# Kernel optimization log

Hardware: AMD Instinct MI355X
Metric: run time of the kernel (lower is better)

The kernel has to match this reference:

```python
import jax, jax.numpy as jnp
import numpy as np
import math

BLK_NUM, BLK_SIZE = 128, 8
DIM, N_HEADS, N_KV_HEADS = 1024, 16, 4
HEAD_DIM = DIM // N_HEADS            # 64
HIDDEN = 64 * ((DIM + 63) // 64)     # 1024 (FeedForward hidden_dim)
BATCH = 4
SEQ = BLK_NUM * BLK_SIZE             # 1024
EPS = 1e-6
ROPE_THETA = 10000.0


def setup_inputs() -> dict:
    key = jax.random.key(0)
    ks = jax.random.split(key, 12)
    std = 1.0 / math.sqrt(DIM)
    f32 = jnp.float32
    inp = {
        "x":   jax.random.normal(ks[0], (BATCH, SEQ, DIM), f32),
        "vec": jax.random.normal(ks[1], (BATCH, BLK_NUM, DIM), f32),
        "wq": jax.random.normal(ks[2], (N_HEADS * HEAD_DIM, DIM), f32) * std,
        "wk": jax.random.normal(ks[3], (N_KV_HEADS * HEAD_DIM, DIM), f32) * std,
        "wv": jax.random.normal(ks[4], (N_KV_HEADS * HEAD_DIM, DIM), f32) * std,
        "wo": jax.random.normal(ks[5], (DIM, N_HEADS * HEAD_DIM), f32) * std,
        "w1": jax.random.normal(ks[6], (HIDDEN, DIM), f32) * std,
        "w2": jax.random.normal(ks[7], (DIM, HIDDEN), f32) * std,
        "w3": jax.random.normal(ks[8], (HIDDEN, DIM), f32) * std,
        "mod_attn_w": jax.random.normal(ks[9], (3 * DIM, DIM), f32) * std,
        "mod_attn_b": jnp.zeros((3 * DIM,), f32),
        "mod_ffn_w":  jax.random.normal(ks[10], (3 * DIM, DIM), f32) * std,
        "mod_ffn_b":  jnp.zeros((3 * DIM,), f32),
        "norm1_w": jnp.ones((DIM,), f32),
        "norm2_w": jnp.ones((DIM,), f32),
    }
    # rotary tables (equivalent to llama-style precompute_freqs_cis, theta=rope_scaling)
    inv_freq = 1.0 / (ROPE_THETA ** (jnp.arange(0, HEAD_DIM, 2, dtype=f32) / HEAD_DIM))
    angles = jnp.outer(jnp.arange(SEQ, dtype=f32), inv_freq)  # (SEQ, HEAD_DIM//2)
    inp["freqs_cos"] = jnp.cos(angles)
    inp["freqs_sin"] = jnp.sin(angles)
    return inp


def _rmsnorm(x, w):
    return x * jax.lax.rsqrt(jnp.mean(x * x, axis=-1, keepdims=True) + EPS) * w


def _rope(x, cos, sin):
    # x: (B, L, H, Dh); pairs are adjacent dims, matching view_as_complex on (..., Dh//2, 2)
    x1, x2 = x[..., 0::2], x[..., 1::2]
    c, s = cos[None, :, None, :], sin[None, :, None, :]
    return jnp.stack([x1 * c - x2 * s, x1 * s + x2 * c], axis=-1).reshape(x.shape)


def _modulate(vec, w, b):
    # adaLN: silu(vec) -> 3*dim, chunked into shift/scale/gate, one vector per block
    out = jax.nn.silu(vec) @ w.T + b
    shift, scale, gate = jnp.split(out, 3, axis=-1)
    rep = lambda t: jnp.repeat(t, BLK_SIZE, axis=1)  # (B, M, D) -> (B, L, D)
    return rep(shift), rep(scale), rep(gate)


def _block_attention(xn, freqs_cos, freqs_sin, wq, wk, wv, wo):
    B, L, _ = xn.shape
    q = (xn @ wq.T).reshape(B, L, N_HEADS, HEAD_DIM)
    k = (xn @ wk.T).reshape(B, L, N_KV_HEADS, HEAD_DIM)
    v = (xn @ wv.T).reshape(B, L, N_KV_HEADS, HEAD_DIM)
    q = _rope(q, freqs_cos, freqs_sin)
    k = _rope(k, freqs_cos, freqs_sin)
    g = N_HEADS // N_KV_HEADS  # GQA expansion (enable_gqa in flex_attention)
    k = jnp.repeat(k, g, axis=2)
    v = jnp.repeat(v, g, axis=2)
    q, k, v = (t.transpose(0, 2, 1, 3) for t in (q, k, v))  # (B, H, L, Dh)
    scores = jnp.einsum('bhqd,bhkd->bhqk', q, k) * (1.0 / math.sqrt(HEAD_DIM))
    blk = jnp.arange(L) // BLK_SIZE
    allow = blk[:, None] >= blk[None, :]  # block-causal: full attn within block, causal across blocks
    scores = jnp.where(allow, scores, jnp.asarray(-1e9, scores.dtype))
    probs = jax.nn.softmax(scores, axis=-1)
    out = jnp.einsum('bhqk,bhkd->bhqd', probs, v)
    out = out.transpose(0, 2, 1, 3).reshape(B, L, N_HEADS * HEAD_DIM)
    return out @ wo.T


def reference(x, vec, freqs_cos, freqs_sin, wq, wk, wv, wo, w1, w2, w3,
              mod_attn_w, mod_attn_b, mod_ffn_w, mod_ffn_b, norm1_w, norm2_w):
    sh_a, sc_a, gt_a = _modulate(vec, mod_attn_w, mod_attn_b)
    xn = _rmsnorm(x, norm1_w) * (1.0 + sc_a) + sh_a
    h = x + gt_a * _block_attention(xn, freqs_cos, freqs_sin, wq, wk, wv, wo)
    sh_f, sc_f, gt_f = _modulate(vec, mod_ffn_w, mod_ffn_b)
    hn = _rmsnorm(h, norm2_w) * (1.0 + sc_f) + sh_f
    ffn = (jax.nn.silu(hn @ w1.T) * (hn @ w3.T)) @ w2.T  # SwiGLU FeedForward
    return h + gt_f * ffn
```

## Files before the change

kernel.cpp:

```cpp
#include <hip/hip_runtime.h>
#include <math.h>

#define SEQ 1024
#define DIM 1024

using short8 = __attribute__((ext_vector_type(8))) short;
using f32x4  = __attribute__((ext_vector_type(4))) float;

__device__ __forceinline__ unsigned short f2bf(float f) {
  unsigned int u = __float_as_uint(f);
  u = (u + 0x7FFFu + ((u >> 16) & 1u)) >> 16;
  return (unsigned short)u;
}
__device__ __forceinline__ float bf2f(unsigned short h) {
  return __uint_as_float(((unsigned int)h) << 16);
}
__device__ __forceinline__ void load16_lds(const unsigned short* g, unsigned short* l) {
  __builtin_amdgcn_global_load_lds((const __attribute__((address_space(1))) void*)g,
                                   (__attribute__((address_space(3))) void*)l, 16, 0, 0);
}

struct CastArgs {
  const float* src[9];
  unsigned short* dst[9];
  int n[9];
  int ilv[9];
};
__global__ __launch_bounds__(256) void cast_weights(CastArgs a) {
  int r = blockIdx.y;
  int i4 = (blockIdx.x * 256 + threadIdx.x) * 4;
  if (i4 >= a.n[r]) return;
  const float4 v = *(const float4*)(a.src[r] + i4);
  ushort4 o;
  o.x = f2bf(v.x); o.y = f2bf(v.y); o.z = f2bf(v.z); o.w = f2bf(v.w);
  size_t di = i4;
  if (a.ilv[r]) di = (size_t)((i4 >> 10) * 2 + (a.ilv[r] - 1)) * 1024 + (i4 & 1023);
  *(ushort4*)(a.dst[r] + di) = o;
}

__global__ __launch_bounds__(256) void silu_cast(const float* __restrict__ v,
                                                 unsigned short* __restrict__ o, int n) {
  int i4 = (blockIdx.x * 256 + threadIdx.x) * 4;
  if (i4 >= n) return;
  float4 x = *(const float4*)(v + i4);
  ushort4 r;
  r.x = f2bf(x.x / (1.0f + expf(-x.x)));
  r.y = f2bf(x.y / (1.0f + expf(-x.y)));
  r.z = f2bf(x.z / (1.0f + expf(-x.z)));
  r.w = f2bf(x.w / (1.0f + expf(-x.w)));
  *(ushort4*)(o + i4) = r;
}

template<int EPI>
__global__ __launch_bounds__(256) void mfma_gemm(
    const unsigned short* __restrict__ A, const unsigned short* __restrict__ W,
    int M, int N, int K,
    float* __restrict__ outF, unsigned short* __restrict__ outBF,
    const float* __restrict__ aux1,
    const float* __restrict__ aux2,
    const float* __restrict__ fc, const float* __restrict__ fs)
{
  __shared__ unsigned short sA[2][128 * 64];
  __shared__ unsigned short sB[2][64 * 64];
  const int tid = threadIdx.x;
  const int lane = tid & 63;
  const int wv = tid >> 6;
  const int wr = wv >> 1;
  const int wc = wv & 1;
  const int rowBlk = blockIdx.y * 128;
  const int colBlk = blockIdx.x * 64;
  const int q = lane >> 4;
  const int cl = lane & 15;

  f32x4 acc[4][2] = {};

  auto stage = [&](int bf, int k0) {
#pragma unroll
    for (int j = 0; j < 4; ++j) {
      int slot = j * 256 + tid;
      int row = slot >> 3;
      int cg = (slot & 7) ^ (row & 7);
      load16_lds(A + (size_t)(rowBlk + row) * K + k0 + cg * 8, &sA[bf][slot * 8]);
    }
#pragma unroll
    for (int j = 0; j < 2; ++j) {
      int slot = j * 256 + tid;
      int row = slot >> 3;
      int cg = (slot & 7) ^ (row & 7);
      load16_lds(W + (size_t)(colBlk + row) * K + k0 + cg * 8, &sB[bf][slot * 8]);
    }
  };

  auto compute = [&](int bf) {
    short8 af[4][2], bfr[2][2];
#pragma unroll
    for (int t = 0; t < 4; ++t) {
      int row = wr * 64 + t * 16 + cl;
#pragma unroll
      for (int s = 0; s < 2; ++s)
        af[t][s] = *(const short8*)&sA[bf][row * 64 + (((s * 4 + q) ^ (cl & 7)) * 8)];
    }
#pragma unroll
    for (int t = 0; t < 2; ++t) {
      int row = wc * 32 + t * 16 + cl;
#pragma unroll
      for (int s = 0; s < 2; ++s)
        bfr[t][s] = *(const short8*)&sB[bf][row * 64 + (((s * 4 + q) ^ (cl & 7)) * 8)];
    }
#pragma unroll
    for (int s = 0; s < 2; ++s)
#pragma unroll
      for (int tm = 0; tm < 4; ++tm)
#pragma unroll
        for (int tn = 0; tn < 2; ++tn)
          acc[tm][tn] = __builtin_amdgcn_mfma_f32_16x16x32_bf16(af[tm][s], bfr[tn][s], acc[tm][tn], 0, 0, 0);
  };

  stage(0, 0);
  int cur = 0;
  for (int k0 = 64; k0 < K; k0 += 64) {
    __syncthreads();
    stage(cur ^ 1, k0);
    compute(cur);
    cur ^= 1;
  }
  __syncthreads();
  compute(cur);

#pragma unroll
  for (int tm = 0; tm < 4; ++tm) {
#pragma unroll
    for (int tn = 0; tn < 2; ++tn) {
      const int col = colBlk + wc * 32 + tn * 16 + cl;
#pragma unroll
      for (int r = 0; r < 4; ++r) {
        const int row = rowBlk + wr * 64 + tm * 16 + q * 4 + r;
        float v = acc[tm][tn][r];
        if constexpr (EPI == 0) {
          float other = __shfl_xor(v, 1);
          if (col < 1280) {
            int s = row & (SEQ - 1);
            int t = (col & 63) >> 1;
            float cv = fc[s * 32 + t], sv = fs[s * 32 + t];
            v = ((col & 1) == 0) ? (v * cv - other * sv) : (other * sv + v * cv);
          }
          outBF[(size_t)row * N + col] = f2bf(v);
        } else if constexpr (EPI == 1) {
          float bb = (col < 3072) ? aux1[col] : aux2[col - 3072];
          outF[(size_t)row * N + col] = v + bb;
        } else if constexpr (EPI == 2 || EPI == 4) {
          int vr = (row >> 10) * 128 + ((row & (SEQ - 1)) >> 3);
          outF[(size_t)row * N + col] =
              aux1[(size_t)row * N + col] + aux2[(size_t)vr * 6144 + col] * v;
        } else if constexpr (EPI == 3) {
          float other = __shfl_xor(v, 1);
          if ((col & 1) == 0) {
            float g = v / (1.0f + expf(-v)) * other;
            outBF[(size_t)row * 1024 + (col >> 1)] = f2bf(g);
          }
        }
      }
    }
  }
}

__global__ __launch_bounds__(256) void rms_mod(
    const float* __restrict__ X, const float* __restrict__ w,
    const float* __restrict__ mod, int off, unsigned short* __restrict__ out)
{
  const int r = blockIdx.x;
  const int b = r >> 10, s = r & (SEQ - 1);
  const int vr = b * 128 + (s >> 3);
  const size_t base = (size_t)r * DIM;
  float v[4];
  float ss = 0.f;
#pragma unroll
  for (int p = 0; p < 4; ++p) {
    int c = threadIdx.x + p * 256;
    v[p] = X[base + c];
    ss += v[p] * v[p];
  }
#pragma unroll
  for (int o = 1; o < 64; o <<= 1) ss += __shfl_xor(ss, o);
  __shared__ float red[4];
  int lane = threadIdx.x & 63, wvv = threadIdx.x >> 6;
  if (lane == 0) red[wvv] = ss;
  __syncthreads();
  float total = red[0] + red[1] + red[2] + red[3];
  float rn = rsqrtf(total * (1.0f / 1024.0f) + 1e-6f);
  const float* mrow = mod + (size_t)vr * 6144 + off;
#pragma unroll
  for (int p = 0; p < 4; ++p) {
    int c = threadIdx.x + p * 256;
    out[base + c] = f2bf(v[p] * rn * w[c] * (1.0f + mrow[1024 + c]) + mrow[c]);
  }
}

__global__ __launch_bounds__(256) void attn_mfma(
    const unsigned short* __restrict__ QKV, unsigned short* __restrict__ O)
{
  const int bid = blockIdx.x;
  const int pr = bid & 7;
  const int h = (bid >> 3) & 15;
  const int b = bid >> 7;
  const int kvh = h >> 2;
  __shared__ unsigned short sK[64 * 64];
  __shared__ unsigned short sVt[64 * 72];
  __shared__ unsigned short sP[4][16 * 72];
  const int tid = threadIdx.x;
  const int lane = tid & 63;
  const int w = tid >> 6;
  const int q = lane >> 4;
  const int cl = lane & 15;
  const float SCL = 0.125f * 1.44269504f;

  for (int ph = 0; ph < 2; ++ph) {
    const int qt = ph ? (15 - pr) : pr;

    short8 qf[2];
    {
      const size_t qrow = (size_t)(b * SEQ + qt * 64 + w * 16 + cl) * 1536 + h * 64;
#pragma unroll
      for (int s = 0; s < 2; ++s)
        qf[s] = *(const short8*)(QKV + qrow + s * 32 + q * 8);
    }

    f32x4 accO[4] = {};
    float m_r[4], l_r[4];
#pragma unroll
    for (int r = 0; r < 4; ++r) { m_r[r] = -1e30f; l_r[r] = 0.f; }

    for (int kt = 0; kt <= qt; ++kt) {
      __syncthreads();
      {
        int rr = tid >> 3;
        int d0 = (tid & 7) * 8;
#pragma unroll
        for (int ppp = 0; ppp < 2; ++ppp) {
          int key = ppp * 32 + rr;
          const unsigned short* g =
              QKV + (size_t)(b * SEQ + kt * 64 + key) * 1536 + 1024 + kvh * 64 + d0;
          short8 kv = *(const short8*)g;
          *(short8*)(sK + key * 64 + (d0 ^ ((key & 7) * 8))) = kv;
        }
        int d = tid & 63;
        int kg = tid >> 6;
#pragma unroll
        for (int ppp = 0; ppp < 2; ++ppp) {
          int key0 = ppp * 32 + kg * 8;
          unsigned short tmp[8];
#pragma unroll
          for (int j = 0; j < 8; ++j)
            tmp[j] = QKV[(size_t)(b * SEQ + kt * 64 + key0 + j) * 1536 + 1280 + kvh * 64 + d];
          *(short8*)(sVt + d * 72 + key0) = *(const short8*)tmp;
        }
      }
      __syncthreads();

      f32x4 accS[4] = {};
#pragma unroll
      for (int s = 0; s < 2; ++s) {
#pragma unroll
        for (int n = 0; n < 4; ++n) {
          int rowk = n * 16 + cl;
          short8 kf = *(const short8*)(sK + rowk * 64 + ((s * 32 + q * 8) ^ ((cl & 7) * 8)));
          accS[n] = __builtin_amdgcn_mfma_f32_16x16x32_bf16(qf[s], kf, accS[n], 0, 0, 0);
        }
      }

      float sv[4][4];
      const bool diag = (kt == qt);
      const int qblk = w * 2 + (q >> 1);
#pragma unroll
      for (int n = 0; n < 4; ++n) {
        const bool msk = diag && (n * 2 + (cl >> 3)) > qblk;
#pragma unroll
        for (int r = 0; r < 4; ++r)
          sv[n][r] = msk ? -1e30f : accS[n][r] * SCL;
      }

      float alpha[4];
#pragma unroll
      for (int r = 0; r < 4; ++r) {
        float vmax = fmaxf(fmaxf(sv[0][r], sv[1][r]), fmaxf(sv[2][r], sv[3][r]));
        vmax = fmaxf(vmax, __shfl_xor(vmax, 1));
        vmax = fmaxf(vmax, __shfl_xor(vmax, 2));
        vmax = fmaxf(vmax, __shfl_xor(vmax, 4));
        vmax = fmaxf(vmax, __shfl_xor(vmax, 8));
        float mnew = fmaxf(m_r[r], vmax);
        alpha[r] = exp2f(m_r[r] - mnew);
        float rs = 0.f;
#pragma unroll
        for (int n = 0; n < 4; ++n) {
          float pp = exp2f(sv[n][r] - mnew);
          sv[n][r] = pp;
          rs += pp;
        }
        rs += __shfl_xor(rs, 1);
        rs += __shfl_xor(rs, 2);
        rs += __shfl_xor(rs, 4);
        rs += __shfl_xor(rs, 8);
        l_r[r] = l_r[r] * alpha[r] + rs;
        m_r[r] = mnew;
      }

#pragma unroll
      for (int n = 0; n < 4; ++n)
#pragma unroll
        for (int r = 0; r < 4; ++r)
          sP[w][(q * 4 + r) * 72 + n * 16 + cl] = f2bf(sv[n][r]);

#pragma unroll
      for (int dn = 0; dn < 4; ++dn) {
        accO[dn][0] *= alpha[0];
        accO[dn][1] *= alpha[1];
        accO[dn][2] *= alpha[2];
        accO[dn][3] *= alpha[3];
      }

      short8 pf[2];
      pf[0] = *(const short8*)(&sP[w][cl * 72 + q * 8]);
      pf[1] = *(const short8*)(&sP[w][cl * 72 + 32 + q * 8]);
#pragma unroll
      for (int dn = 0; dn < 4; ++dn) {
#pragma unroll
        for (int s = 0; s < 2; ++s) {
          short8 vf = *(const short8*)(sVt + (dn * 16 + cl) * 72 + s * 32 + q * 8);
          accO[dn] = __builtin_amdgcn_mfma_f32_16x16x32_bf16(pf[s], vf, accO[dn], 0, 0, 0);
        }
      }
    }

    float invl[4];
#pragma unroll
    for (int r = 0; r < 4; ++r) invl[r] = 1.0f / l_r[r];
#pragma unroll
    for (int dn = 0; dn < 4; ++dn)
#pragma unroll
      for (int r = 0; r < 4; ++r) {
        int row = b * SEQ + qt * 64 + w * 16 + q * 4 + r;
        O[(size_t)row * DIM + h * 64 + dn * 16 + cl] = f2bf(accO[dn][r] * invl[r]);
      }
    __syncthreads();
  }
}

extern "C" void kernel_launch(void* const* d_in, const int* in_sizes, int n_in,
                              void* d_out, int out_size, void* d_ws, size_t ws_size,
                              hipStream_t stream)
{
  const float* x   = (const float*)d_in[0];
  const float* vec = (const float*)d_in[1];
  const float* wq  = (const float*)d_in[2];
  const float* wk  = (const float*)d_in[3];
  const float* wv  = (const float*)d_in[4];
  const float* wo  = (const float*)d_in[5];
  const float* w1  = (const float*)d_in[6];
  const float* w2  = (const float*)d_in[7];
  const float* w3  = (const float*)d_in[8];
  const float* maw = (const float*)d_in[9];
  const float* mab = (const float*)d_in[10];
  const float* mfw = (const float*)d_in[11];
  const float* mfb = (const float*)d_in[12];
  const float* n1w = (const float*)d_in[13];
  const float* n2w = (const float*)d_in[14];
  const float* fc  = (const float*)d_in[15];
  const float* fs  = (const float*)d_in[16];

  char* p = (char*)d_ws;
  auto takeU = [&](size_t elems) { unsigned short* r = (unsigned short*)p; p += elems * 2; return r; };
  auto takeF = [&](size_t elems) { float* r = (float*)p; p += elems * 4; return r; };

  unsigned short* WQKV = takeU((size_t)1536 * 1024);
  unsigned short* WOb  = takeU((size_t)1024 * 1024);
  unsigned short* W13  = takeU((size_t)2048 * 1024);
  unsigned short* W2b  = takeU((size_t)1024 * 1024);
  unsigned short* WM   = takeU((size_t)6144 * 1024);
  unsigned short* SVEC = takeU((size_t)512 * 1024);
  float* MOD  = takeF((size_t)512 * 6144);
  float* H    = takeF((size_t)4096 * 1024);
  unsigned short* XNb  = takeU((size_t)4096 * 1024);
  unsigned short* QKVb = takeU((size_t)4096 * 1536);
  unsigned short* AOb  = takeU((size_t)4096 * 1024);
  unsigned short* HNb  = takeU((size_t)4096 * 1024);
  unsigned short* Gb  = AOb;

  dim3 blk(256);

  CastArgs ca;
  ca.src[0] = wq;  ca.dst[0] = WQKV;                    ca.n[0] = 1024 * 1024; ca.ilv[0] = 0;
  ca.src[1] = wk;  ca.dst[1] = WQKV + 1024 * 1024;      ca.n[1] = 256 * 1024;  ca.ilv[1] = 0;
  ca.src[2] = wv;  ca.dst[2] = WQKV + 1280 * 1024;      ca.n[2] = 256 * 1024;  ca.ilv[2] = 0;
  ca.src[3] = wo;  ca.dst[3] = WOb;                     ca.n[3] = 1024 * 1024; ca.ilv[3] = 0;
  ca.src[4] = w1;  ca.dst[4] = W13;                     ca.n[4] = 1024 * 1024; ca.ilv[4] = 1;
  ca.src[5] = w3;  ca.dst[5] = W13;                     ca.n[5] = 1024 * 1024; ca.ilv[5] = 2;
  ca.src[6] = w2;  ca.dst[6] = W2b;                     ca.n[6] = 1024 * 1024; ca.ilv[6] = 0;
  ca.src[7] = maw; ca.dst[7] = WM;                      ca.n[7] = 3072 * 1024; ca.ilv[7] = 0;
  ca.src[8] = mfw; ca.dst[8] = WM + (size_t)3072 * 1024; ca.n[8] = 3072 * 1024; ca.ilv[8] = 0;
  cast_weights<<<dim3(3072, 9), blk, 0, stream>>>(ca);

  silu_cast<<<512, blk, 0, stream>>>(vec, SVEC, 512 * 1024);

  mfma_gemm<1><<<dim3(96, 4), blk, 0, stream>>>(SVEC, WM, 512, 6144, 1024,
      MOD, nullptr, mab, mfb, nullptr, nullptr);

  rms_mod<<<4096, blk, 0, stream>>>(x, n1w, MOD, 0, XNb);

  mfma_gemm<0><<<dim3(24, 32), blk, 0, stream>>>(XNb, WQKV, 4096, 1536, 1024,
      nullptr, QKVb, nullptr, nullptr, fc, fs);

  attn_mfma<<<512, blk, 0, stream>>>(QKVb, AOb);

  mfma_gemm<2><<<dim3(16, 32), blk, 0, stream>>>(AOb, WOb, 4096, 1024, 1024,
      H, nullptr, x, MOD + 2048, nullptr, nullptr);

  rms_mod<<<4096, blk, 0, stream>>>(H, n2w, MOD, 3072, HNb);

  mfma_gemm<3><<<dim3(32, 32), blk, 0, stream>>>(HNb, W13, 4096, 2048, 1024,
      nullptr, Gb, nullptr, nullptr, nullptr, nullptr);

  mfma_gemm<4><<<dim3(16, 32), blk, 0, stream>>>(Gb, W2b, 4096, 1024, 1024,
      (float*)d_out, nullptr, H, MOD + 5120, nullptr, nullptr);
}
```

Before: 326.7 us.

## Load GEMM A fragments directly to registers and prefetch attention K/V tiles

The GEMM stops staging the A tile through LDS. Each wave now loads its A fragments straight from global memory into registers, double-buffered across two unrolled k-steps, while B is still staged in LDS. The attention kernel prefetches the next K/V tile into registers while computing on the current one, and drops the trailing barrier at the end of each phase. This cuts LDS traffic and hides global-load latency, at the cost of more register pressure and uncoalesced row-strided A loads. The GEMM loop also assumes K is a multiple of 128.

```diff
diff --git a/kernel.cpp b/kernel.cpp
--- a/kernel.cpp
+++ b/kernel.cpp
@@ -60,7 +60,6 @@
     const float* __restrict__ aux2,
     const float* __restrict__ fc, const float* __restrict__ fs)
 {
-  __shared__ unsigned short sA[2][128 * 64];
   __shared__ unsigned short sB[2][64 * 64];
   const int tid = threadIdx.x;
   const int lane = tid & 63;
@@ -74,14 +73,12 @@
 
   f32x4 acc[4][2] = {};
 
-  auto stage = [&](int bf, int k0) {
-#pragma unroll
-    for (int j = 0; j < 4; ++j) {
-      int slot = j * 256 + tid;
-      int row = slot >> 3;
-      int cg = (slot & 7) ^ (row & 7);
-      load16_lds(A + (size_t)(rowBlk + row) * K + k0 + cg * 8, &sA[bf][slot * 8]);
-    }
+  const unsigned short* Abase[4];
+#pragma unroll
+  for (int t = 0; t < 4; ++t)
+    Abase[t] = A + (size_t)(rowBlk + wr * 64 + t * 16 + cl) * K + q * 8;
+
+  auto stageB = [&](int bf, int k0) {
 #pragma unroll
     for (int j = 0; j < 2; ++j) {
       int slot = j * 256 + tid;
@@ -91,41 +88,40 @@
     }
   };
 
-  auto compute = [&](int bf) {
-    short8 af[4][2], bfr[2][2];
-#pragma unroll
-    for (int t = 0; t < 4; ++t) {
-      int row = wr * 64 + t * 16 + cl;
-#pragma unroll
-      for (int s = 0; s < 2; ++s)
-        af[t][s] = *(const short8*)&sA[bf][row * 64 + (((s * 4 + q) ^ (cl & 7)) * 8)];
-    }
-#pragma unroll
-    for (int t = 0; t < 2; ++t) {
-      int row = wc * 32 + t * 16 + cl;
-#pragma unroll
-      for (int s = 0; s < 2; ++s)
-        bfr[t][s] = *(const short8*)&sB[bf][row * 64 + (((s * 4 + q) ^ (cl & 7)) * 8)];
-    }
-#pragma unroll
-    for (int s = 0; s < 2; ++s)
-#pragma unroll
-      for (int tm = 0; tm < 4; ++tm)
-#pragma unroll
-        for (int tn = 0; tn < 2; ++tn)
-          acc[tm][tn] = __builtin_amdgcn_mfma_f32_16x16x32_bf16(af[tm][s], bfr[tn][s], acc[tm][tn], 0, 0, 0);
-  };
-
-  stage(0, 0);
-  int cur = 0;
-  for (int k0 = 64; k0 < K; k0 += 64) {
+  short8 afE[4][2], afO[4][2];
+#define LOADA(dst, k0v)                                        \
+  _Pragma("unroll") for (int t = 0; t < 4; ++t)                \
+    _Pragma("unroll") for (int s = 0; s < 2; ++s)              \
+      dst[t][s] = *(const short8*)(Abase[t] + (k0v) + s * 32);
+
+#define COMPUTE(af, bf)                                                          \
+  {                                                                              \
+    short8 bfr[2][2];                                                            \
+    _Pragma("unroll") for (int t = 0; t < 2; ++t) {                              \
+      int rowb = wc * 32 + t * 16 + cl;                                          \
+      _Pragma("unroll") for (int s = 0; s < 2; ++s)                              \
+        bfr[t][s] = *(const short8*)&sB[bf][rowb * 64 + (((s * 4 + q) ^ (cl & 7)) * 8)]; \
+    }                                                                            \
+    _Pragma("unroll") for (int s = 0; s < 2; ++s)                                \
+      _Pragma("unroll") for (int tm = 0; tm < 4; ++tm)                           \
+        _Pragma("unroll") for (int tn = 0; tn < 2; ++tn)                         \
+          acc[tm][tn] = __builtin_amdgcn_mfma_f32_16x16x32_bf16(af[tm][s], bfr[tn][s], acc[tm][tn], 0, 0, 0); \
+  }
+
+  stageB(0, 0);
+  LOADA(afE, 0);
+  for (int k0 = 0; k0 < K; k0 += 128) {
     __syncthreads();
-    stage(cur ^ 1, k0);
-    compute(cur);
-    cur ^= 1;
-  }
-  __syncthreads();
-  compute(cur);
+    stageB(1, k0 + 64);
+    LOADA(afO, k0 + 64);
+    COMPUTE(afE, 0);
+    __syncthreads();
+    if (k0 + 128 < K) {
+      stageB(0, k0 + 128);
+      LOADA(afE, k0 + 128);
+    }
+    COMPUTE(afO, 1);
+  }
 
 #pragma unroll
   for (int tm = 0; tm < 4; ++tm) {
@@ -214,6 +210,36 @@
   const int cl = lane & 15;
   const float SCL = 0.125f * 1.44269504f;
 
+  const int krr = tid >> 3;
+  const int kd0 = (tid & 7) * 8;
+  const int vd  = tid & 63;
+  const int vkg = tid >> 6;
+
+  short8 kreg[2];
+  unsigned short vreg[2][8];
+
+  auto loadKV = [&](int kt) {
+    const size_t rb = (size_t)(b * SEQ + kt * 64);
+#pragma unroll
+    for (int ppp = 0; ppp < 2; ++ppp)
+      kreg[ppp] = *(const short8*)(QKV + (rb + ppp * 32 + krr) * 1536 + 1024 + kvh * 64 + kd0);
+#pragma unroll
+    for (int ppp = 0; ppp < 2; ++ppp)
+#pragma unroll
+      for (int j = 0; j < 8; ++j)
+        vreg[ppp][j] = QKV[(rb + ppp * 32 + vkg * 8 + j) * 1536 + 1280 + kvh * 64 + vd];
+  };
+  auto writeKV = [&]() {
+#pragma unroll
+    for (int ppp = 0; ppp < 2; ++ppp) {
+      int key = ppp * 32 + krr;
+      *(short8*)(sK + key * 64 + (kd0 ^ ((key & 7) * 8))) = kreg[ppp];
+    }
+#pragma unroll
+    for (int ppp = 0; ppp < 2; ++ppp)
+      *(short8*)(sVt + vd * 72 + ppp * 32 + vkg * 8) = *(const short8*)vreg[ppp];
+  };
+
   for (int ph = 0; ph < 2; ++ph) {
     const int qt = ph ? (15 - pr) : pr;
 
@@ -230,32 +256,12 @@
 #pragma unroll
     for (int r = 0; r < 4; ++r) { m_r[r] = -1e30f; l_r[r] = 0.f; }
 
+    loadKV(0);
     for (int kt = 0; kt <= qt; ++kt) {
       __syncthreads();
-      {
-        int rr = tid >> 3;
-        int d0 = (tid & 7) * 8;
-#pragma unroll
-        for (int ppp = 0; ppp < 2; ++ppp) {
-          int key = ppp * 32 + rr;
-          const unsigned short* g =
-              QKV + (size_t)(b * SEQ + kt * 64 + key) * 1536 + 1024 + kvh * 64 + d0;
-          short8 kv = *(const short8*)g;
-          *(short8*)(sK + key * 64 + (d0 ^ ((key & 7) * 8))) = kv;
-        }
-        int d = tid & 63;
-        int kg = tid >> 6;
-#pragma unroll
-        for (int ppp = 0; ppp < 2; ++ppp) {
-          int key0 = ppp * 32 + kg * 8;
-          unsigned short tmp[8];
-#pragma unroll
-          for (int j = 0; j < 8; ++j)
-            tmp[j] = QKV[(size_t)(b * SEQ + kt * 64 + key0 + j) * 1536 + 1280 + kvh * 64 + d];
-          *(short8*)(sVt + d * 72 + key0) = *(const short8*)tmp;
-        }
-      }
+      writeKV();
       __syncthreads();
+      if (kt < qt) loadKV(kt + 1);
 
       f32x4 accS[4] = {};
 #pragma unroll
@@ -341,7 +347,6 @@
         int row = b * SEQ + qt * 64 + w * 16 + q * 4 + r;
         O[(size_t)row * DIM + h * 64 + dn * 16 + cl] = f2bf(accO[dn][r] * invl[r]);
       }
-    __syncthreads();
   }
 }
 
```

Result: slower. 433.8 us (+32.8%).
